# Optimization experiments

Measured on AMD Instinct MI355X. Metric: run time of the kernel, lower is better.

Reference implementation:

```python
import jax, jax.numpy as jnp
import numpy as np

N_NODES = 100000
N_EDGES = 1600000
N_GRAPHS = 512
F_IN = 128
HID = 128
N_CLS = 10


def setup_inputs() -> dict:
    key = jax.random.key(0)
    ks = jax.random.split(key, 8)
    s = 1.0 / np.sqrt(HID)
    x = jax.random.normal(ks[0], (N_NODES, F_IN), dtype=jnp.float32)
    edge_index = jax.random.randint(ks[1], (2, N_EDGES), 0, N_NODES, dtype=jnp.int64)
    batch = jnp.sort(jax.random.randint(ks[2], (N_NODES,), 0, N_GRAPHS, dtype=jnp.int64))
    W0 = jax.random.normal(ks[3], (F_IN, HID), dtype=jnp.float32) * s
    W1 = jax.random.normal(ks[4], (HID, HID), dtype=jnp.float32) * s
    W2 = jax.random.normal(ks[5], (HID, HID), dtype=jnp.float32) * s
    Wl = jax.random.normal(ks[6], (HID, N_CLS), dtype=jnp.float32) * s
    return {
        'x': x, 'edge_index': edge_index, 'batch': batch,
        'W0': W0, 'b0': jnp.zeros((HID,), jnp.float32),
        'W1': W1, 'b1': jnp.zeros((HID,), jnp.float32),
        'W2': W2, 'b2': jnp.zeros((HID,), jnp.float32),
        'Wl': Wl, 'bl': jnp.zeros((N_CLS,), jnp.float32),
    }


def reference(x, edge_index, batch, W0, b0, W1, b1, W2, b2, Wl, bl):
    N = x.shape[0]
    # GCN: add self-loops, symmetric normalization D^-1/2 (A+I) D^-1/2
    loops = jnp.arange(N, dtype=edge_index.dtype)
    row = jnp.concatenate([edge_index[0], loops])  # source
    col = jnp.concatenate([edge_index[1], loops])  # target
    deg = jax.ops.segment_sum(jnp.ones_like(col, dtype=x.dtype), col, num_segments=N)
    dinv = jax.lax.rsqrt(jnp.maximum(deg, 1.0))  # deg >= 1 after self-loops
    norm = dinv[row] * dinv[col]  # [E+N]

    def gcn(h, W, b):
        h = h @ W                       # [N, H] linear transform first (fewer edge flops)
        msg = h[row] * norm[:, None]    # gather + normalize
        return jax.ops.segment_sum(msg, col, num_segments=N) + b  # scatter-add

    h = jax.nn.relu(gcn(x, W0, b0))
    h = jax.nn.relu(gcn(h, W1, b1))
    h = jax.nn.relu(gcn(h, W2, b2))

    # global_mean_pool over graphs
    counts = jax.ops.segment_sum(jnp.ones((N,), x.dtype), batch, num_segments=N_GRAPHS)
    pooled = jax.ops.segment_sum(h, batch, num_segments=N_GRAPHS) / jnp.maximum(counts, 1.0)[:, None]
    return pooled @ Wl + bl
```

## Files before the change

kernel.cpp:

```cpp
#include <hip/hip_runtime.h>
#include <hip/hip_bf16.h>

#define ELL_D 64

typedef __attribute__((ext_vector_type(8))) short short8;
typedef __attribute__((ext_vector_type(4))) float f32x4;

__device__ __forceinline__ unsigned short f2bf(float f) {
    __hip_bfloat16 h = __float2bfloat16(f);
    return *(unsigned short*)&h;
}
__device__ __forceinline__ float bf2f(unsigned short u) {
    unsigned int v = ((unsigned int)u) << 16;
    return __uint_as_float(v);
}


__device__ __forceinline__ void gemm_body(int bid, const float* __restrict__ H,
                                          const float* __restrict__ W, unsigned short* __restrict__ A,
                                          int N, float4* wl4) {
    int tid = threadIdx.x;
    const float4* __restrict__ W4 = (const float4*)W;
    int tc = tid & 15;
    int tr = tid >> 4;
    int rbase = bid * 64 + tr * 4;

    const float4* __restrict__ H4 = (const float4*)H;
    float acc[4][8] = {};
    int r[4];
#pragma unroll
    for (int j = 0; j < 4; j++) {
        int rr = rbase + j;
        r[j] = (rr < N) ? rr : (N - 1);
    }

    for (int p = 0; p < 2; p++) {
        if (p) __syncthreads();
#pragma unroll
        for (int i = 0; i < 8; i++) wl4[i * 256 + tid] = W4[p * 2048 + i * 256 + tid];
        __syncthreads();
#pragma unroll 4
        for (int k4 = 0; k4 < 16; k4++) {
            union { float4 v; float f[4]; } hu[4];
#pragma unroll
            for (int j = 0; j < 4; j++) hu[j].v = H4[r[j] * 32 + p * 16 + k4];
#pragma unroll
            for (int kk = 0; kk < 4; kk++) {
                float4 w0 = wl4[(k4 * 4 + kk) * 32 + tc];
                float4 w1 = wl4[(k4 * 4 + kk) * 32 + 16 + tc];
#pragma unroll
                for (int j = 0; j < 4; j++) {
                    float h = hu[j].f[kk];
                    acc[j][0] = fmaf(h, w0.x, acc[j][0]);
                    acc[j][1] = fmaf(h, w0.y, acc[j][1]);
                    acc[j][2] = fmaf(h, w0.z, acc[j][2]);
                    acc[j][3] = fmaf(h, w0.w, acc[j][3]);
                    acc[j][4] = fmaf(h, w1.x, acc[j][4]);
                    acc[j][5] = fmaf(h, w1.y, acc[j][5]);
                    acc[j][6] = fmaf(h, w1.z, acc[j][6]);
                    acc[j][7] = fmaf(h, w1.w, acc[j][7]);
                }
            }
        }
    }

    ushort4* __restrict__ A4 = (ushort4*)A;
#pragma unroll
    for (int j = 0; j < 4; j++) {
        int rr = rbase + j;
        if (rr < N) {
            A4[rr * 32 + tc]      = make_ushort4(f2bf(acc[j][0]), f2bf(acc[j][1]), f2bf(acc[j][2]), f2bf(acc[j][3]));
            A4[rr * 32 + 16 + tc] = make_ushort4(f2bf(acc[j][4]), f2bf(acc[j][5]), f2bf(acc[j][6]), f2bf(acc[j][7]));
        }
    }
}

__device__ __forceinline__ void fill_body(int bid, const int* __restrict__ col, const int* __restrict__ row,
                                          int* __restrict__ cnt, int* __restrict__ ell, int E) {
    int t = bid * 256 + threadIdx.x;
    int base = t * 4;
    if (base + 4 <= E) {
        int4 c4 = *(const int4*)(col + base);
        int4 r4 = *(const int4*)(row + base);
        int p0 = atomicAdd(&cnt[c4.x], 1) & 63;
        int p1 = atomicAdd(&cnt[c4.y], 1) & 63;
        int p2 = atomicAdd(&cnt[c4.z], 1) & 63;
        int p3 = atomicAdd(&cnt[c4.w], 1) & 63;
        ell[c4.x * ELL_D + p0] = r4.x;
        ell[c4.y * ELL_D + p1] = r4.y;
        ell[c4.z * ELL_D + p2] = r4.z;
        ell[c4.w * ELL_D + p3] = r4.w;
    } else {
        for (int e = base; e < E; e++) {
            int c = col[e];
            int pos = atomicAdd(&cnt[c], 1) & 63;
            ell[c * ELL_D + pos] = row[e];
        }
    }
}

__global__ __launch_bounds__(256) void k_fused_gemm_fill(const float* __restrict__ H, const float* __restrict__ W,
                                                         unsigned short* __restrict__ A,
                                                         const int* __restrict__ col, const int* __restrict__ row,
                                                         int* __restrict__ cnt, int* __restrict__ ell,
                                                         int N, int E, int gb, int fb) {
    __shared__ float4 wl4[2048];
    int half = blockIdx.x >> 1;
    if (!(blockIdx.x & 1)) {
        if (half < gb) gemm_body(half, H, W, A, N, wl4);
    } else {
        if (half < fb) fill_body(half, col, row, cnt, ell, E);
    }
}

__global__ __launch_bounds__(256) void k_prep_wt(const float* __restrict__ W1, const float* __restrict__ W2,
                                                 unsigned short* __restrict__ WT1, unsigned short* __restrict__ WT2) {
    const float* W = blockIdx.x ? W2 : W1;
    unsigned short* WT = blockIdx.x ? WT2 : WT1;
    for (int i = threadIdx.x; i < 16384; i += 256) {
        int c = i >> 7, k = i & 127;
        WT[i] = f2bf(W[k * 128 + c]);
    }
}

__global__ __launch_bounds__(256) void k_dinv_scaleA(const int* __restrict__ cnt, float* __restrict__ dinv,
                                                     unsigned short* __restrict__ A, int N) {
    int node = blockIdx.x * 8 + (threadIdx.x >> 5);
    int li = threadIdx.x & 31;
    if (node >= N) return;
    float dn = 1.0f / sqrtf((float)(cnt[node] + 1));
    if (li == 0) dinv[node] = dn;
    ushort4* Ap = (ushort4*)A + (size_t)node * 32 + li;
    ushort4 v = *Ap;
    v.x = f2bf(bf2f(v.x) * dn);
    v.y = f2bf(bf2f(v.y) * dn);
    v.z = f2bf(bf2f(v.z) * dn);
    v.w = f2bf(bf2f(v.w) * dn);
    *Ap = v;
}


__global__ __launch_bounds__(256) void k_gemm_mfma(const unsigned short* __restrict__ H,
                                                   const unsigned short* __restrict__ WT,
                                                   const float* __restrict__ dinv,
                                                   unsigned short* __restrict__ A, int N) {
    __shared__ float ep[4 * 16 * 132];
    int tid = threadIdx.x, w = tid >> 6, l = tid & 63;
    int rbase = blockIdx.x * 64 + w * 16;
    int lrow = l & 15, lk = l >> 4;

    int r = rbase + lrow;
    if (r >= N) r = N - 1;
    const short8* __restrict__ Hp = (const short8*)(H + (size_t)r * 128);
    short8 af[4];
#pragma unroll
    for (int kc = 0; kc < 4; kc++) af[kc] = Hp[kc * 4 + lk];

    f32x4 acc[8];
#pragma unroll
    for (int t = 0; t < 8; t++) {
        f32x4 a = {0.f, 0.f, 0.f, 0.f};
        const short8* __restrict__ Wp = (const short8*)(WT + (size_t)(t * 16 + lrow) * 128);
#pragma unroll
        for (int kc = 0; kc < 4; kc++) {
            short8 bf = Wp[kc * 4 + lk];
            a = __builtin_amdgcn_mfma_f32_16x16x32_bf16(af[kc], bf, a, 0, 0, 0);
        }
        acc[t] = a;
    }

    float* base = ep + w * 2112;
#pragma unroll
    for (int t = 0; t < 8; t++)
#pragma unroll
        for (int j = 0; j < 4; j++)
            base[(4 * lk + j) * 132 + t * 16 + lrow] = acc[t][j];
    __syncthreads();

    int row16 = l >> 2, c0 = (l & 3) * 32;
    int orow = rbase + row16;
    if (orow < N) {
        float dn = dinv[orow];
        const float* src = base + row16 * 132 + c0;
        unsigned short* dst = A + (size_t)orow * 128 + c0;
#pragma unroll
        for (int q = 0; q < 4; q++) {
            union { short8 s; unsigned short u[8]; } pk;
#pragma unroll
            for (int e = 0; e < 8; e++) pk.u[e] = f2bf(src[q * 8 + e] * dn);
            *(short8*)(dst + q * 8) = pk.s;
        }
    }
}


__global__ __launch_bounds__(256) void k_agg(const unsigned short* __restrict__ A, const int* __restrict__ cnt,
                                             const int* __restrict__ ell, const float* __restrict__ dinv,
                                             const float* __restrict__ bias, unsigned short* __restrict__ Bout, int N) {
    int wid = blockIdx.x * 4 + (threadIdx.x >> 6);
    int lane = threadIdx.x & 63;
    if (wid >= N) return;
    int hi = lane >> 5, li = lane & 31;
    const ushort4* __restrict__ A4 = (const ushort4*)A;
    int deg = cnt[wid];
    float dn = dinv[wid];
    const int* __restrict__ lst = ell + wid * ELL_D;

    int total = deg + 1;
    int pairs = (total + 1) >> 1;

    float4 a0 = {0,0,0,0}, a1 = {0,0,0,0}, a2 = {0,0,0,0}, a3 = {0,0,0,0};
    int i = 0;
    for (; i + 4 <= pairs; i += 4) {
        int s0 = 2 * i + hi, s1 = s0 + 2, s2 = s0 + 4, s3 = s0 + 6;
        int e0 = (s0 < deg) ? lst[s0] : wid;
        int e1 = (s1 < deg) ? lst[s1] : wid;
        int e2 = (s2 < deg) ? lst[s2] : wid;
        int e3 = (s3 < deg) ? lst[s3] : wid;
        float m0 = (s0 < total) ? 1.f : 0.f;
        float m1 = (s1 < total) ? 1.f : 0.f;
        float m2 = (s2 < total) ? 1.f : 0.f;
        float m3 = (s3 < total) ? 1.f : 0.f;
        ushort4 v0 = A4[e0 * 32 + li];
        ushort4 v1 = A4[e1 * 32 + li];
        ushort4 v2 = A4[e2 * 32 + li];
        ushort4 v3 = A4[e3 * 32 + li];
        a0.x = fmaf(bf2f(v0.x), m0, a0.x); a0.y = fmaf(bf2f(v0.y), m0, a0.y);
        a0.z = fmaf(bf2f(v0.z), m0, a0.z); a0.w = fmaf(bf2f(v0.w), m0, a0.w);
        a1.x = fmaf(bf2f(v1.x), m1, a1.x); a1.y = fmaf(bf2f(v1.y), m1, a1.y);
        a1.z = fmaf(bf2f(v1.z), m1, a1.z); a1.w = fmaf(bf2f(v1.w), m1, a1.w);
        a2.x = fmaf(bf2f(v2.x), m2, a2.x); a2.y = fmaf(bf2f(v2.y), m2, a2.y);
        a2.z = fmaf(bf2f(v2.z), m2, a2.z); a2.w = fmaf(bf2f(v2.w), m2, a2.w);
        a3.x = fmaf(bf2f(v3.x), m3, a3.x); a3.y = fmaf(bf2f(v3.y), m3, a3.y);
        a3.z = fmaf(bf2f(v3.z), m3, a3.z); a3.w = fmaf(bf2f(v3.w), m3, a3.w);
    }
    for (; i < pairs; i++) {
        int s0 = 2 * i + hi;
        int e0 = (s0 < deg) ? lst[s0] : wid;
        float m0 = (s0 < total) ? 1.f : 0.f;
        ushort4 v0 = A4[e0 * 32 + li];
        a0.x = fmaf(bf2f(v0.x), m0, a0.x); a0.y = fmaf(bf2f(v0.y), m0, a0.y);
        a0.z = fmaf(bf2f(v0.z), m0, a0.z); a0.w = fmaf(bf2f(v0.w), m0, a0.w);
    }
    a0.x = (a0.x + a1.x) + (a2.x + a3.x);
    a0.y = (a0.y + a1.y) + (a2.y + a3.y);
    a0.z = (a0.z + a1.z) + (a2.z + a3.z);
    a0.w = (a0.w + a1.w) + (a2.w + a3.w);
    a0.x += __shfl_xor(a0.x, 32, 64);
    a0.y += __shfl_xor(a0.y, 32, 64);
    a0.z += __shfl_xor(a0.z, 32, 64);
    a0.w += __shfl_xor(a0.w, 32, 64);

    if (hi == 0) {
        const float4* __restrict__ b4 = (const float4*)bias;
        float4 bb = b4[li];
        ushort4 o;
        o.x = f2bf(fmaxf(fmaf(a0.x, dn, bb.x), 0.f));
        o.y = f2bf(fmaxf(fmaf(a0.y, dn, bb.y), 0.f));
        o.z = f2bf(fmaxf(fmaf(a0.z, dn, bb.z), 0.f));
        o.w = f2bf(fmaxf(fmaf(a0.w, dn, bb.w), 0.f));
        ((ushort4*)Bout)[wid * 32 + li] = o;
    }
}


__global__ __launch_bounds__(512) void k_pool(const unsigned short* __restrict__ B, const int* __restrict__ batch,
                                              const float* __restrict__ Wl, const float* __restrict__ bl,
                                              float* __restrict__ out, int N) {
    int g = blockIdx.x;
    int tid = threadIdx.x;
    int k = tid & 127, h = tid >> 7;
    __shared__ int se[2];
    __shared__ float red[4][128];
    if (tid < 2) {
        int target = g + tid;
        int lo = 0, hi = N;
        while (lo < hi) {
            int mid = (lo + hi) >> 1;
            if (batch[mid] < target) lo = mid + 1; else hi = mid;
        }
        se[tid] = lo;
    }
    __syncthreads();
    int start = se[0], end = se[1];
    float s = 0.f;
    for (int n = start + h; n < end; n += 4) s += bf2f(B[n * 128 + k]);
    red[h][k] = s;
    __syncthreads();
    if (h == 0) {
        float tot = red[0][k] + red[1][k] + red[2][k] + red[3][k];
        int cg = end - start;
        red[0][k] = tot / (float)(cg > 1 ? cg : 1);
    }
    __syncthreads();
    if (tid < 10) {
        float o = bl[tid];
        for (int j = 0; j < 128; j++) o = fmaf(red[0][j], Wl[j * 10 + tid], o);
        out[g * 10 + tid] = o;
    }
}


extern "C" void kernel_launch(void* const* d_in, const int* in_sizes, int n_in,
                              void* d_out, int out_size, void* d_ws, size_t ws_size,
                              hipStream_t stream) {
    const float* x  = (const float*)d_in[0];
    const int* eidx = (const int*)d_in[1];
    const int* batch = (const int*)d_in[2];
    const float* W0 = (const float*)d_in[3];
    const float* b0 = (const float*)d_in[4];
    const float* W1 = (const float*)d_in[5];
    const float* b1 = (const float*)d_in[6];
    const float* W2 = (const float*)d_in[7];
    const float* b2 = (const float*)d_in[8];
    const float* Wl = (const float*)d_in[9];
    const float* bl = (const float*)d_in[10];

    int N = in_sizes[0] / 128;
    int E = in_sizes[1] / 2;
    int G = out_size / 10;
    const int* row = eidx;
    const int* col = eidx + E;

    char* w = (char*)d_ws;
    auto carve = [&](size_t bytes) -> void* {
        void* p = (void*)w;
        w += (bytes + 511) & ~(size_t)511;
        return p;
    };
    unsigned short* A  = (unsigned short*)carve((size_t)N * 128 * 2);
    unsigned short* Bb = (unsigned short*)carve((size_t)N * 128 * 2);
    int*   cnt  = (int*)carve((size_t)N * 4);
    float* dinv = (float*)carve((size_t)N * 4);
    int*   ell  = (int*)carve((size_t)N * ELL_D * 4);
    unsigned short* WT1 = (unsigned short*)carve(16384 * 2);
    unsigned short* WT2 = (unsigned short*)carve(16384 * 2);

    int gb = (N + 63) / 64;
    int ft = (E + 3) / 4;
    int fb = (ft + 255) / 256;
    int M  = (gb > fb) ? gb : fb;

    hipMemsetAsync(cnt, 0, (size_t)N * 4, stream);
    k_prep_wt<<<2, 256, 0, stream>>>(W1, W2, WT1, WT2);
    k_fused_gemm_fill<<<2 * M, 256, 0, stream>>>(x, W0, A, col, row, cnt, ell, N, E, gb, fb);
    k_dinv_scaleA<<<(N + 7) / 8, 256, 0, stream>>>(cnt, dinv, A, N);

    int ab = (N + 3) / 4;
    int mb = (N + 63) / 64;
    k_agg<<<ab, 256, 0, stream>>>(A, cnt, ell, dinv, b0, Bb, N);
    k_gemm_mfma<<<mb, 256, 0, stream>>>(Bb, WT1, dinv, A, N);
    k_agg<<<ab, 256, 0, stream>>>(A, cnt, ell, dinv, b1, Bb, N);
    k_gemm_mfma<<<mb, 256, 0, stream>>>(Bb, WT2, dinv, A, N);
    k_agg<<<ab, 256, 0, stream>>>(A, cnt, ell, dinv, b2, Bb, N);
    k_pool<<<G, 512, 0, stream>>>(Bb, batch, Wl, bl, (float*)d_out, N);
}
```

Before: 411.9 us.

## Partition ELL fill by destination range across block groups for atomic locality

```diff
diff --git a/kernel.cpp b/kernel.cpp
--- a/kernel.cpp
+++ b/kernel.cpp
@@ -2,6 +2,8 @@
 #include <hip/hip_bf16.h>
 
 #define ELL_D 64
+#define FK 128
+#define FBT (8 * FK)
 
 typedef __attribute__((ext_vector_type(8))) short short8;
 typedef __attribute__((ext_vector_type(4))) float f32x4;
@@ -75,41 +77,49 @@
     }
 }
 
-__device__ __forceinline__ void fill_body(int bid, const int* __restrict__ col, const int* __restrict__ row,
-                                          int* __restrict__ cnt, int* __restrict__ ell, int E) {
-    int t = bid * 256 + threadIdx.x;
-    int base = t * 4;
-    if (base + 4 <= E) {
-        int4 c4 = *(const int4*)(col + base);
-        int4 r4 = *(const int4*)(row + base);
-        int p0 = atomicAdd(&cnt[c4.x], 1) & 63;
-        int p1 = atomicAdd(&cnt[c4.y], 1) & 63;
-        int p2 = atomicAdd(&cnt[c4.z], 1) & 63;
-        int p3 = atomicAdd(&cnt[c4.w], 1) & 63;
-        ell[c4.x * ELL_D + p0] = r4.x;
-        ell[c4.y * ELL_D + p1] = r4.y;
-        ell[c4.z * ELL_D + p2] = r4.z;
-        ell[c4.w * ELL_D + p3] = r4.w;
+
+__device__ __forceinline__ void fill_own_body(int b, const int* __restrict__ col, const int* __restrict__ row,
+                                              int* __restrict__ cnt, int* __restrict__ ell, int E, int N) {
+    int r = b & 7, k = b >> 3;
+    int nr = (N + 7) / 8;
+    int lo = r * nr;
+    int hi = lo + nr; if (hi > N) hi = N;
+    int tid = threadIdx.x;
+    int E4 = E >> 2;
+    int chunk = (E4 + FK - 1) / FK;
+    int q0 = k * chunk;
+    int q1 = q0 + chunk; if (q1 > E4) q1 = E4;
+    const int4* __restrict__ c4p = (const int4*)col;
+    const int4* __restrict__ r4p = (const int4*)row;
+    for (int q = q0 + tid; q < q1; q += 256) {
+        int4 c4 = c4p[q];
+        int4 r4 = r4p[q];
+        if (c4.x >= lo && c4.x < hi) { int p = atomicAdd(&cnt[c4.x], 1) & 63; ell[c4.x * ELL_D + p] = r4.x; }
+        if (c4.y >= lo && c4.y < hi) { int p = atomicAdd(&cnt[c4.y], 1) & 63; ell[c4.y * ELL_D + p] = r4.y; }
+        if (c4.z >= lo && c4.z < hi) { int p = atomicAdd(&cnt[c4.z], 1) & 63; ell[c4.z * ELL_D + p] = r4.z; }
+        if (c4.w >= lo && c4.w < hi) { int p = atomicAdd(&cnt[c4.w], 1) & 63; ell[c4.w * ELL_D + p] = r4.w; }
+    }
+    if (k == FK - 1) {
+        int rem = E & 3;
+        if (tid < rem) {
+            int e = E4 * 4 + tid;
+            int c = col[e];
+            if (c >= lo && c < hi) { int p = atomicAdd(&cnt[c], 1) & 63; ell[c * ELL_D + p] = row[e]; }
+        }
+    }
+}
+
+__global__ __launch_bounds__(256) void k_fused(const float* __restrict__ H, const float* __restrict__ W,
+                                               unsigned short* __restrict__ A,
+                                               const int* __restrict__ col, const int* __restrict__ row,
+                                               int* __restrict__ cnt, int* __restrict__ ell,
+                                               int N, int E, int gb) {
+    __shared__ float4 wl4[2048];
+    if (blockIdx.x < FBT) {
+        fill_own_body(blockIdx.x, col, row, cnt, ell, E, N);
     } else {
-        for (int e = base; e < E; e++) {
-            int c = col[e];
-            int pos = atomicAdd(&cnt[c], 1) & 63;
-            ell[c * ELL_D + pos] = row[e];
-        }
-    }
-}
-
-__global__ __launch_bounds__(256) void k_fused_gemm_fill(const float* __restrict__ H, const float* __restrict__ W,
-                                                         unsigned short* __restrict__ A,
-                                                         const int* __restrict__ col, const int* __restrict__ row,
-                                                         int* __restrict__ cnt, int* __restrict__ ell,
-                                                         int N, int E, int gb, int fb) {
-    __shared__ float4 wl4[2048];
-    int half = blockIdx.x >> 1;
-    if (!(blockIdx.x & 1)) {
-        if (half < gb) gemm_body(half, H, W, A, N, wl4);
-    } else {
-        if (half < fb) fill_body(half, col, row, cnt, ell, E);
+        int gbid = blockIdx.x - FBT;
+        if (gbid < gb) gemm_body(gbid, H, W, A, N, wl4);
     }
 }
 
@@ -185,10 +195,10 @@
         unsigned short* dst = A + (size_t)orow * 128 + c0;
 #pragma unroll
         for (int q = 0; q < 4; q++) {
-            union { short8 s; unsigned short u[8]; } pk;
+            union { short8 s8; unsigned short u[8]; } pk;
 #pragma unroll
             for (int e = 0; e < 8; e++) pk.u[e] = f2bf(src[q * 8 + e] * dn);
-            *(short8*)(dst + q * 8) = pk.s;
+            *(short8*)(dst + q * 8) = pk.s8;
         }
     }
 }
@@ -337,13 +347,10 @@
     unsigned short* WT2 = (unsigned short*)carve(16384 * 2);
 
     int gb = (N + 63) / 64;
-    int ft = (E + 3) / 4;
-    int fb = (ft + 255) / 256;
-    int M  = (gb > fb) ? gb : fb;
 
     hipMemsetAsync(cnt, 0, (size_t)N * 4, stream);
     k_prep_wt<<<2, 256, 0, stream>>>(W1, W2, WT1, WT2);
-    k_fused_gemm_fill<<<2 * M, 256, 0, stream>>>(x, W0, A, col, row, cnt, ell, N, E, gb, fb);
+    k_fused<<<FBT + gb, 256, 0, stream>>>(x, W0, A, col, row, cnt, ell, N, E, gb);
     k_dinv_scaleA<<<(N + 7) / 8, 256, 0, stream>>>(cnt, dinv, A, N);
 
     int ab = (N + 3) / 4;
```

Measured after the change: 428.2 us. +4.0%, slower.

## Fuse aggregation with next-layer MFMA GEMM and pad ELL lists with sentinel rows

Applied to the files above, without the earlier changes.

```diff
diff --git a/kernel.cpp b/kernel.cpp
--- a/kernel.cpp
+++ b/kernel.cpp
@@ -74,6 +74,7 @@
         }
     }
 }
+
 
 __device__ __forceinline__ void fill_body(int bid, const int* __restrict__ col, const int* __restrict__ row,
                                           int* __restrict__ cnt, int* __restrict__ ell, int E) {
@@ -99,11 +100,11 @@
     }
 }
 
-__global__ __launch_bounds__(256) void k_fused_gemm_fill(const float* __restrict__ H, const float* __restrict__ W,
-                                                         unsigned short* __restrict__ A,
-                                                         const int* __restrict__ col, const int* __restrict__ row,
-                                                         int* __restrict__ cnt, int* __restrict__ ell,
-                                                         int N, int E, int gb, int fb) {
+__global__ __launch_bounds__(256) void k_fused(const float* __restrict__ H, const float* __restrict__ W,
+                                               unsigned short* __restrict__ A,
+                                               const int* __restrict__ col, const int* __restrict__ row,
+                                               int* __restrict__ cnt, int* __restrict__ ell,
+                                               int N, int E, int gb, int fb) {
     __shared__ float4 wl4[2048];
     int half = blockIdx.x >> 1;
     if (!(blockIdx.x & 1)) {
@@ -123,44 +124,128 @@
     }
 }
 
-__global__ __launch_bounds__(256) void k_dinv_scaleA(const int* __restrict__ cnt, float* __restrict__ dinv,
-                                                     unsigned short* __restrict__ A, int N) {
+
+__global__ __launch_bounds__(256) void k_scaleA_pad(const int* __restrict__ cnt, float* __restrict__ dinv,
+                                                    unsigned short* __restrict__ A1, unsigned short* __restrict__ A2,
+                                                    int* __restrict__ ell, int N) {
     int node = blockIdx.x * 8 + (threadIdx.x >> 5);
     int li = threadIdx.x & 31;
-    if (node >= N) return;
-    float dn = 1.0f / sqrtf((float)(cnt[node] + 1));
-    if (li == 0) dinv[node] = dn;
-    ushort4* Ap = (ushort4*)A + (size_t)node * 32 + li;
-    ushort4 v = *Ap;
-    v.x = f2bf(bf2f(v.x) * dn);
-    v.y = f2bf(bf2f(v.y) * dn);
-    v.z = f2bf(bf2f(v.z) * dn);
-    v.w = f2bf(bf2f(v.w) * dn);
-    *Ap = v;
-}
-
-
-__global__ __launch_bounds__(256) void k_gemm_mfma(const unsigned short* __restrict__ H,
-                                                   const unsigned short* __restrict__ WT,
-                                                   const float* __restrict__ dinv,
-                                                   unsigned short* __restrict__ A, int N) {
-    __shared__ float ep[4 * 16 * 132];
+    if (node < N) {
+        int deg = cnt[node];
+        float dn = 1.0f / sqrtf((float)(deg + 1));
+        if (deg > 63) deg = 63;
+        if (li == 0) dinv[node] = dn;
+        ushort4* Ap = (ushort4*)A1 + (size_t)node * 32 + li;
+        ushort4 v = *Ap;
+        v.x = f2bf(bf2f(v.x) * dn);
+        v.y = f2bf(bf2f(v.y) * dn);
+        v.z = f2bf(bf2f(v.z) * dn);
+        v.w = f2bf(bf2f(v.w) * dn);
+        *Ap = v;
+        int pend = (deg + 4) & ~3;
+        int* er = ell + (size_t)node * ELL_D;
+        if (li == 0) er[deg] = node;
+        else if (li < 4 && deg + li < pend) er[deg + li] = N;
+    }
+    if (blockIdx.x == 0) {
+        int t = threadIdx.x;
+        if (t < 64) {
+            ushort4 z = make_ushort4(0, 0, 0, 0);
+            if (t < 32) ((ushort4*)A1)[(size_t)N * 32 + t] = z;
+            else        ((ushort4*)A2)[(size_t)N * 32 + (t - 32)] = z;
+        }
+    }
+}
+
+
+__device__ __forceinline__ void agg_core(const ushort4* __restrict__ A4r, const int* __restrict__ cnt,
+                                         const int* __restrict__ ell, int n, int hi, int li,
+                                         float4& a0, float4& a1) {
+    int deg = cnt[n];
+    if (deg > 63) deg = 63;
+    int nq = (deg + 4) >> 2;
+    const int4* __restrict__ l4 = (const int4*)(ell + (size_t)n * ELL_D);
+    int q = 0;
+    for (; q + 2 <= nq; q += 2) {
+        int4 qa = l4[q], qb = l4[q + 1];
+        int e0 = hi ? qa.y : qa.x, e1 = hi ? qa.w : qa.z;
+        int e2 = hi ? qb.y : qb.x, e3 = hi ? qb.w : qb.z;
+        ushort4 v0 = A4r[(size_t)e0 * 32 + li];
+        ushort4 v1 = A4r[(size_t)e1 * 32 + li];
+        ushort4 v2 = A4r[(size_t)e2 * 32 + li];
+        ushort4 v3 = A4r[(size_t)e3 * 32 + li];
+        a0.x += bf2f(v0.x) + bf2f(v1.x);
+        a0.y += bf2f(v0.y) + bf2f(v1.y);
+        a0.z += bf2f(v0.z) + bf2f(v1.z);
+        a0.w += bf2f(v0.w) + bf2f(v1.w);
+        a1.x += bf2f(v2.x) + bf2f(v3.x);
+        a1.y += bf2f(v2.y) + bf2f(v3.y);
+        a1.z += bf2f(v2.z) + bf2f(v3.z);
+        a1.w += bf2f(v2.w) + bf2f(v3.w);
+    }
+    if (q < nq) {
+        int4 qa = l4[q];
+        int e0 = hi ? qa.y : qa.x, e1 = hi ? qa.w : qa.z;
+        ushort4 v0 = A4r[(size_t)e0 * 32 + li];
+        ushort4 v1 = A4r[(size_t)e1 * 32 + li];
+        a0.x += bf2f(v0.x) + bf2f(v1.x);
+        a0.y += bf2f(v0.y) + bf2f(v1.y);
+        a0.z += bf2f(v0.z) + bf2f(v1.z);
+        a0.w += bf2f(v0.w) + bf2f(v1.w);
+    }
+}
+
+
+__global__ __launch_bounds__(256) void k_agg_gemm(const unsigned short* __restrict__ Ain,
+                                                  const int* __restrict__ cnt, const int* __restrict__ ell,
+                                                  const float* __restrict__ dinv, const float* __restrict__ bias,
+                                                  const unsigned short* __restrict__ WT,
+                                                  unsigned short* __restrict__ Aout, int N) {
+    __shared__ char lds[33792];
+    unsigned short* hb = (unsigned short*)lds;
+    float* ep = (float*)lds;
     int tid = threadIdx.x, w = tid >> 6, l = tid & 63;
-    int rbase = blockIdx.x * 64 + w * 16;
-    int lrow = l & 15, lk = l >> 4;
-
-    int r = rbase + lrow;
-    if (r >= N) r = N - 1;
-    const short8* __restrict__ Hp = (const short8*)(H + (size_t)r * 128);
+    int hi = l >> 5, li = l & 31;
+    int rbase = blockIdx.x * 64;
+    const ushort4* __restrict__ A4r = (const ushort4*)Ain;
+    float4 bb = ((const float4*)bias)[li];
+
+    for (int it = 0; it < 16; ++it) {
+        int lrow = w * 16 + it;
+        int n = rbase + lrow;
+        float4 a0 = {0, 0, 0, 0}, a1 = {0, 0, 0, 0};
+        if (n < N) {
+            agg_core(A4r, cnt, ell, n, hi, li, a0, a1);
+            a0.x += a1.x; a0.y += a1.y; a0.z += a1.z; a0.w += a1.w;
+            a0.x += __shfl_xor(a0.x, 32, 64);
+            a0.y += __shfl_xor(a0.y, 32, 64);
+            a0.z += __shfl_xor(a0.z, 32, 64);
+            a0.w += __shfl_xor(a0.w, 32, 64);
+        }
+        if (hi == 0) {
+            float dn = (n < N) ? dinv[n] : 0.f;
+            ushort4 o;
+            o.x = f2bf(fmaxf(fmaf(a0.x, dn, bb.x), 0.f));
+            o.y = f2bf(fmaxf(fmaf(a0.y, dn, bb.y), 0.f));
+            o.z = f2bf(fmaxf(fmaf(a0.z, dn, bb.z), 0.f));
+            o.w = f2bf(fmaxf(fmaf(a0.w, dn, bb.w), 0.f));
+            *(ushort4*)(hb + (size_t)lrow * 136 + li * 4) = o;
+        }
+    }
+    __syncthreads();
+
+    int lrow16 = l & 15, lk = l >> 4;
+    const unsigned short* hrow = hb + (size_t)(w * 16 + lrow16) * 136;
     short8 af[4];
 #pragma unroll
-    for (int kc = 0; kc < 4; kc++) af[kc] = Hp[kc * 4 + lk];
+    for (int kc = 0; kc < 4; kc++) af[kc] = *(const short8*)(hrow + kc * 32 + lk * 8);
+    __syncthreads();
 
     f32x4 acc[8];
 #pragma unroll
     for (int t = 0; t < 8; t++) {
         f32x4 a = {0.f, 0.f, 0.f, 0.f};
-        const short8* __restrict__ Wp = (const short8*)(WT + (size_t)(t * 16 + lrow) * 128);
+        const short8* __restrict__ Wp = (const short8*)(WT + (size_t)(t * 16 + lrow16) * 128);
 #pragma unroll
         for (int kc = 0; kc < 4; kc++) {
             short8 bf = Wp[kc * 4 + lk];
@@ -174,86 +259,44 @@
     for (int t = 0; t < 8; t++)
 #pragma unroll
         for (int j = 0; j < 4; j++)
-            base[(4 * lk + j) * 132 + t * 16 + lrow] = acc[t][j];
+            base[(4 * lk + j) * 132 + t * 16 + lrow16] = acc[t][j];
     __syncthreads();
 
     int row16 = l >> 2, c0 = (l & 3) * 32;
-    int orow = rbase + row16;
+    int orow = rbase + w * 16 + row16;
     if (orow < N) {
         float dn = dinv[orow];
         const float* src = base + row16 * 132 + c0;
-        unsigned short* dst = A + (size_t)orow * 128 + c0;
+        unsigned short* dst = Aout + (size_t)orow * 128 + c0;
 #pragma unroll
         for (int q = 0; q < 4; q++) {
-            union { short8 s; unsigned short u[8]; } pk;
+            union { short8 s8; unsigned short u[8]; } pk;
 #pragma unroll
             for (int e = 0; e < 8; e++) pk.u[e] = f2bf(src[q * 8 + e] * dn);
-            *(short8*)(dst + q * 8) = pk.s;
-        }
-    }
-}
-
-
-__global__ __launch_bounds__(256) void k_agg(const unsigned short* __restrict__ A, const int* __restrict__ cnt,
+            *(short8*)(dst + q * 8) = pk.s8;
+        }
+    }
+}
+
+
+__global__ __launch_bounds__(256) void k_agg(const unsigned short* __restrict__ Ain, const int* __restrict__ cnt,
                                              const int* __restrict__ ell, const float* __restrict__ dinv,
                                              const float* __restrict__ bias, unsigned short* __restrict__ Bout, int N) {
     int wid = blockIdx.x * 4 + (threadIdx.x >> 6);
     int lane = threadIdx.x & 63;
     if (wid >= N) return;
     int hi = lane >> 5, li = lane & 31;
-    const ushort4* __restrict__ A4 = (const ushort4*)A;
-    int deg = cnt[wid];
-    float dn = dinv[wid];
-    const int* __restrict__ lst = ell + wid * ELL_D;
-
-    int total = deg + 1;
-    int pairs = (total + 1) >> 1;
-
-    float4 a0 = {0,0,0,0}, a1 = {0,0,0,0}, a2 = {0,0,0,0}, a3 = {0,0,0,0};
-    int i = 0;
-    for (; i + 4 <= pairs; i += 4) {
-        int s0 = 2 * i + hi, s1 = s0 + 2, s2 = s0 + 4, s3 = s0 + 6;
-        int e0 = (s0 < deg) ? lst[s0] : wid;
-        int e1 = (s1 < deg) ? lst[s1] : wid;
-        int e2 = (s2 < deg) ? lst[s2] : wid;
-        int e3 = (s3 < deg) ? lst[s3] : wid;
-        float m0 = (s0 < total) ? 1.f : 0.f;
-        float m1 = (s1 < total) ? 1.f : 0.f;
-        float m2 = (s2 < total) ? 1.f : 0.f;
-        float m3 = (s3 < total) ? 1.f : 0.f;
-        ushort4 v0 = A4[e0 * 32 + li];
-        ushort4 v1 = A4[e1 * 32 + li];
-        ushort4 v2 = A4[e2 * 32 + li];
-        ushort4 v3 = A4[e3 * 32 + li];
-        a0.x = fmaf(bf2f(v0.x), m0, a0.x); a0.y = fmaf(bf2f(v0.y), m0, a0.y);
-        a0.z = fmaf(bf2f(v0.z), m0, a0.z); a0.w = fmaf(bf2f(v0.w), m0, a0.w);
-        a1.x = fmaf(bf2f(v1.x), m1, a1.x); a1.y = fmaf(bf2f(v1.y), m1, a1.y);
-        a1.z = fmaf(bf2f(v1.z), m1, a1.z); a1.w = fmaf(bf2f(v1.w), m1, a1.w);
-        a2.x = fmaf(bf2f(v2.x), m2, a2.x); a2.y = fmaf(bf2f(v2.y), m2, a2.y);
-        a2.z = fmaf(bf2f(v2.z), m2, a2.z); a2.w = fmaf(bf2f(v2.w), m2, a2.w);
-        a3.x = fmaf(bf2f(v3.x), m3, a3.x); a3.y = fmaf(bf2f(v3.y), m3, a3.y);
-        a3.z = fmaf(bf2f(v3.z), m3, a3.z); a3.w = fmaf(bf2f(v3.w), m3, a3.w);
-    }
-    for (; i < pairs; i++) {
-        int s0 = 2 * i + hi;
-        int e0 = (s0 < deg) ? lst[s0] : wid;
-        float m0 = (s0 < total) ? 1.f : 0.f;
-        ushort4 v0 = A4[e0 * 32 + li];
-        a0.x = fmaf(bf2f(v0.x), m0, a0.x); a0.y = fmaf(bf2f(v0.y), m0, a0.y);
-        a0.z = fmaf(bf2f(v0.z), m0, a0.z); a0.w = fmaf(bf2f(v0.w), m0, a0.w);
-    }
-    a0.x = (a0.x + a1.x) + (a2.x + a3.x);
-    a0.y = (a0.y + a1.y) + (a2.y + a3.y);
-    a0.z = (a0.z + a1.z) + (a2.z + a3.z);
-    a0.w = (a0.w + a1.w) + (a2.w + a3.w);
+    const ushort4* __restrict__ A4r = (const ushort4*)Ain;
+    float4 a0 = {0, 0, 0, 0}, a1 = {0, 0, 0, 0};
+    agg_core(A4r, cnt, ell, wid, hi, li, a0, a1);
+    a0.x += a1.x; a0.y += a1.y; a0.z += a1.z; a0.w += a1.w;
     a0.x += __shfl_xor(a0.x, 32, 64);
     a0.y += __shfl_xor(a0.y, 32, 64);
     a0.z += __shfl_xor(a0.z, 32, 64);
     a0.w += __shfl_xor(a0.w, 32, 64);
-
     if (hi == 0) {
-        const float4* __restrict__ b4 = (const float4*)bias;
-        float4 bb = b4[li];
+        float dn = dinv[wid];
+        float4 bb = ((const float4*)bias)[li];
         ushort4 o;
         o.x = f2bf(fmaxf(fmaf(a0.x, dn, bb.x), 0.f));
         o.y = f2bf(fmaxf(fmaf(a0.y, dn, bb.y), 0.f));
@@ -328,7 +371,8 @@
         w += (bytes + 511) & ~(size_t)511;
         return p;
     };
-    unsigned short* A  = (unsigned short*)carve((size_t)N * 128 * 2);
+    unsigned short* A1 = (unsigned short*)carve((size_t)(N + 1) * 128 * 2);
+    unsigned short* A2 = (unsigned short*)carve((size_t)(N + 1) * 128 * 2);
     unsigned short* Bb = (unsigned short*)carve((size_t)N * 128 * 2);
     int*   cnt  = (int*)carve((size_t)N * 4);
     float* dinv = (float*)carve((size_t)N * 4);
@@ -343,15 +387,12 @@
 
     hipMemsetAsync(cnt, 0, (size_t)N * 4, stream);
     k_prep_wt<<<2, 256, 0, stream>>>(W1, W2, WT1, WT2);
-    k_fused_gemm_fill<<<2 * M, 256, 0, stream>>>(x, W0, A, col, row, cnt, ell, N, E, gb, fb);
-    k_dinv_scaleA<<<(N + 7) / 8, 256, 0, stream>>>(cnt, dinv, A, N);
-
-    int ab = (N + 3) / 4;
+    k_fused<<<2 * M, 256, 0, stream>>>(x, W0, A1, col, row, cnt, ell, N, E, gb, fb);
+    k_scaleA_pad<<<(N + 7) / 8, 256, 0, stream>>>(cnt, dinv, A1, A2, ell, N);
+
     int mb = (N + 63) / 64;
-    k_agg<<<ab, 256, 0, stream>>>(A, cnt, ell, dinv, b0, Bb, N);
-    k_gemm_mfma<<<mb, 256, 0, stream>>>(Bb, WT1, dinv, A, N);
-    k_agg<<<ab, 256, 0, stream>>>(A, cnt, ell, dinv, b1, Bb, N);
-    k_gemm_mfma<<<mb, 256, 0, stream>>>(Bb, WT2, dinv, A, N);
-    k_agg<<<ab, 256, 0, stream>>>(A, cnt, ell, dinv, b2, Bb, N);
+    k_agg_gemm<<<mb, 256, 0, stream>>>(A1, cnt, ell, dinv, b0, WT1, A2, N);
+    k_agg_gemm<<<mb, 256, 0, stream>>>(A2, cnt, ell, dinv, b1, WT2, A1, N);
+    k_agg<<<(N + 3) / 4, 256, 0, stream>>>(A1, cnt, ell, dinv, b2, Bb, N);
     k_pool<<<G, 512, 0, stream>>>(Bb, batch, Wl, bl, (float*)d_out, N);
 }
```

After: 451.3 us. 9.6% more time.

## Pad ELL rows with self-loop and zero-row sentinel; half-wave-per-node aggregation

Applied to the files above, without the earlier changes.

```diff
diff --git a/kernel.cpp b/kernel.cpp
--- a/kernel.cpp
+++ b/kernel.cpp
@@ -74,6 +74,7 @@
         }
     }
 }
+
 
 __device__ __forceinline__ void fill_body(int bid, const int* __restrict__ col, const int* __restrict__ row,
                                           int* __restrict__ cnt, int* __restrict__ ell, int E) {
@@ -99,11 +100,11 @@
     }
 }
 
-__global__ __launch_bounds__(256) void k_fused_gemm_fill(const float* __restrict__ H, const float* __restrict__ W,
-                                                         unsigned short* __restrict__ A,
-                                                         const int* __restrict__ col, const int* __restrict__ row,
-                                                         int* __restrict__ cnt, int* __restrict__ ell,
-                                                         int N, int E, int gb, int fb) {
+__global__ __launch_bounds__(256) void k_fused(const float* __restrict__ H, const float* __restrict__ W,
+                                               unsigned short* __restrict__ A,
+                                               const int* __restrict__ col, const int* __restrict__ row,
+                                               int* __restrict__ cnt, int* __restrict__ ell,
+                                               int N, int E, int gb, int fb) {
     __shared__ float4 wl4[2048];
     int half = blockIdx.x >> 1;
     if (!(blockIdx.x & 1)) {
@@ -123,20 +124,78 @@
     }
 }
 
-__global__ __launch_bounds__(256) void k_dinv_scaleA(const int* __restrict__ cnt, float* __restrict__ dinv,
-                                                     unsigned short* __restrict__ A, int N) {
+
+__global__ __launch_bounds__(256) void k_scaleA_pad(const int* __restrict__ cnt, float* __restrict__ dinv,
+                                                    unsigned short* __restrict__ A, int* __restrict__ ell, int N) {
     int node = blockIdx.x * 8 + (threadIdx.x >> 5);
     int li = threadIdx.x & 31;
-    if (node >= N) return;
-    float dn = 1.0f / sqrtf((float)(cnt[node] + 1));
-    if (li == 0) dinv[node] = dn;
-    ushort4* Ap = (ushort4*)A + (size_t)node * 32 + li;
-    ushort4 v = *Ap;
-    v.x = f2bf(bf2f(v.x) * dn);
-    v.y = f2bf(bf2f(v.y) * dn);
-    v.z = f2bf(bf2f(v.z) * dn);
-    v.w = f2bf(bf2f(v.w) * dn);
-    *Ap = v;
+    if (node < N) {
+        int deg = cnt[node];
+        float dn = 1.0f / sqrtf((float)(deg + 1));
+        if (deg > 63) deg = 63;
+        if (li == 0) dinv[node] = dn;
+        ushort4* Ap = (ushort4*)A + (size_t)node * 32 + li;
+        ushort4 v = *Ap;
+        v.x = f2bf(bf2f(v.x) * dn);
+        v.y = f2bf(bf2f(v.y) * dn);
+        v.z = f2bf(bf2f(v.z) * dn);
+        v.w = f2bf(bf2f(v.w) * dn);
+        *Ap = v;
+        int pend = (deg + 8) & ~7;
+        if (pend > 64) pend = 64;
+        int* er = ell + (size_t)node * ELL_D;
+        if (li == 0) er[deg] = node;
+        else if (li < 8 && deg + li < pend) er[deg + li] = N;
+    }
+    if (blockIdx.x == 0 && threadIdx.x < 32) {
+        ((ushort4*)A)[(size_t)N * 32 + threadIdx.x] = make_ushort4(0, 0, 0, 0);
+    }
+}
+
+
+__global__ __launch_bounds__(256) void k_agg(const unsigned short* __restrict__ Ain, const int* __restrict__ cnt,
+                                             const int* __restrict__ ell, const float* __restrict__ dinv,
+                                             const float* __restrict__ bias, unsigned short* __restrict__ Bout, int N) {
+    int lane = threadIdx.x & 63;
+    int hi = lane >> 5, li = lane & 31;
+    int n = blockIdx.x * 8 + ((threadIdx.x >> 6) << 1) + hi;
+    if (n >= N) return;
+    const ushort4* __restrict__ A4r = (const ushort4*)Ain;
+    int deg = cnt[n];
+    if (deg > 63) deg = 63;
+    int pend = (deg + 8) & ~7;
+    if (pend > 64) pend = 64;
+    int nq = pend >> 2;
+    const int4* __restrict__ l4 = (const int4*)(ell + (size_t)n * ELL_D);
+
+    float4 a0 = {0, 0, 0, 0}, a1 = {0, 0, 0, 0};
+    for (int q = 0; q < nq; q += 2) {
+        int4 qa = l4[q], qb = l4[q + 1];
+        ushort4 v0 = A4r[(size_t)qa.x * 32 + li];
+        ushort4 v1 = A4r[(size_t)qa.y * 32 + li];
+        ushort4 v2 = A4r[(size_t)qa.z * 32 + li];
+        ushort4 v3 = A4r[(size_t)qa.w * 32 + li];
+        ushort4 v4 = A4r[(size_t)qb.x * 32 + li];
+        ushort4 v5 = A4r[(size_t)qb.y * 32 + li];
+        ushort4 v6 = A4r[(size_t)qb.z * 32 + li];
+        ushort4 v7 = A4r[(size_t)qb.w * 32 + li];
+        a0.x += (bf2f(v0.x) + bf2f(v1.x)) + (bf2f(v2.x) + bf2f(v3.x));
+        a0.y += (bf2f(v0.y) + bf2f(v1.y)) + (bf2f(v2.y) + bf2f(v3.y));
+        a0.z += (bf2f(v0.z) + bf2f(v1.z)) + (bf2f(v2.z) + bf2f(v3.z));
+        a0.w += (bf2f(v0.w) + bf2f(v1.w)) + (bf2f(v2.w) + bf2f(v3.w));
+        a1.x += (bf2f(v4.x) + bf2f(v5.x)) + (bf2f(v6.x) + bf2f(v7.x));
+        a1.y += (bf2f(v4.y) + bf2f(v5.y)) + (bf2f(v6.y) + bf2f(v7.y));
+        a1.z += (bf2f(v4.z) + bf2f(v5.z)) + (bf2f(v6.z) + bf2f(v7.z));
+        a1.w += (bf2f(v4.w) + bf2f(v5.w)) + (bf2f(v6.w) + bf2f(v7.w));
+    }
+    float dn = dinv[n];
+    float4 bb = ((const float4*)bias)[li];
+    ushort4 o;
+    o.x = f2bf(fmaxf(fmaf(a0.x + a1.x, dn, bb.x), 0.f));
+    o.y = f2bf(fmaxf(fmaf(a0.y + a1.y, dn, bb.y), 0.f));
+    o.z = f2bf(fmaxf(fmaf(a0.z + a1.z, dn, bb.z), 0.f));
+    o.w = f2bf(fmaxf(fmaf(a0.w + a1.w, dn, bb.w), 0.f));
+    ((ushort4*)Bout)[(size_t)n * 32 + li] = o;
 }
 
 
@@ -185,81 +244,11 @@
         unsigned short* dst = A + (size_t)orow * 128 + c0;
 #pragma unroll
         for (int q = 0; q < 4; q++) {
-            union { short8 s; unsigned short u[8]; } pk;
+            union { short8 s8; unsigned short u[8]; } pk;
 #pragma unroll
             for (int e = 0; e < 8; e++) pk.u[e] = f2bf(src[q * 8 + e] * dn);
-            *(short8*)(dst + q * 8) = pk.s;
-        }
-    }
-}
-
-
-__global__ __launch_bounds__(256) void k_agg(const unsigned short* __restrict__ A, const int* __restrict__ cnt,
-                                             const int* __restrict__ ell, const float* __restrict__ dinv,
-                                             const float* __restrict__ bias, unsigned short* __restrict__ Bout, int N) {
-    int wid = blockIdx.x * 4 + (threadIdx.x >> 6);
-    int lane = threadIdx.x & 63;
-    if (wid >= N) return;
-    int hi = lane >> 5, li = lane & 31;
-    const ushort4* __restrict__ A4 = (const ushort4*)A;
-    int deg = cnt[wid];
-    float dn = dinv[wid];
-    const int* __restrict__ lst = ell + wid * ELL_D;
-
-    int total = deg + 1;
-    int pairs = (total + 1) >> 1;
-
-    float4 a0 = {0,0,0,0}, a1 = {0,0,0,0}, a2 = {0,0,0,0}, a3 = {0,0,0,0};
-    int i = 0;
-    for (; i + 4 <= pairs; i += 4) {
-        int s0 = 2 * i + hi, s1 = s0 + 2, s2 = s0 + 4, s3 = s0 + 6;
-        int e0 = (s0 < deg) ? lst[s0] : wid;
-        int e1 = (s1 < deg) ? lst[s1] : wid;
-        int e2 = (s2 < deg) ? lst[s2] : wid;
-        int e3 = (s3 < deg) ? lst[s3] : wid;
-        float m0 = (s0 < total) ? 1.f : 0.f;
-        float m1 = (s1 < total) ? 1.f : 0.f;
-        float m2 = (s2 < total) ? 1.f : 0.f;
-        float m3 = (s3 < total) ? 1.f : 0.f;
-        ushort4 v0 = A4[e0 * 32 + li];
-        ushort4 v1 = A4[e1 * 32 + li];
-        ushort4 v2 = A4[e2 * 32 + li];
-        ushort4 v3 = A4[e3 * 32 + li];
-        a0.x = fmaf(bf2f(v0.x), m0, a0.x); a0.y = fmaf(bf2f(v0.y), m0, a0.y);
-        a0.z = fmaf(bf2f(v0.z), m0, a0.z); a0.w = fmaf(bf2f(v0.w), m0, a0.w);
-        a1.x = fmaf(bf2f(v1.x), m1, a1.x); a1.y = fmaf(bf2f(v1.y), m1, a1.y);
-        a1.z = fmaf(bf2f(v1.z), m1, a1.z); a1.w = fmaf(bf2f(v1.w), m1, a1.w);
-        a2.x = fmaf(bf2f(v2.x), m2, a2.x); a2.y = fmaf(bf2f(v2.y), m2, a2.y);
-        a2.z = fmaf(bf2f(v2.z), m2, a2.z); a2.w = fmaf(bf2f(v2.w), m2, a2.w);
-        a3.x = fmaf(bf2f(v3.x), m3, a3.x); a3.y = fmaf(bf2f(v3.y), m3, a3.y);
-        a3.z = fmaf(bf2f(v3.z), m3, a3.z); a3.w = fmaf(bf2f(v3.w), m3, a3.w);
-    }
-    for (; i < pairs; i++) {
-        int s0 = 2 * i + hi;
-        int e0 = (s0 < deg) ? lst[s0] : wid;
-        float m0 = (s0 < total) ? 1.f : 0.f;
-        ushort4 v0 = A4[e0 * 32 + li];
-        a0.x = fmaf(bf2f(v0.x), m0, a0.x); a0.y = fmaf(bf2f(v0.y), m0, a0.y);
-        a0.z = fmaf(bf2f(v0.z), m0, a0.z); a0.w = fmaf(bf2f(v0.w), m0, a0.w);
-    }
-    a0.x = (a0.x + a1.x) + (a2.x + a3.x);
-    a0.y = (a0.y + a1.y) + (a2.y + a3.y);
-    a0.z = (a0.z + a1.z) + (a2.z + a3.z);
-    a0.w = (a0.w + a1.w) + (a2.w + a3.w);
-    a0.x += __shfl_xor(a0.x, 32, 64);
-    a0.y += __shfl_xor(a0.y, 32, 64);
-    a0.z += __shfl_xor(a0.z, 32, 64);
-    a0.w += __shfl_xor(a0.w, 32, 64);
-
-    if (hi == 0) {
-        const float4* __restrict__ b4 = (const float4*)bias;
-        float4 bb = b4[li];
-        ushort4 o;
-        o.x = f2bf(fmaxf(fmaf(a0.x, dn, bb.x), 0.f));
-        o.y = f2bf(fmaxf(fmaf(a0.y, dn, bb.y), 0.f));
-        o.z = f2bf(fmaxf(fmaf(a0.z, dn, bb.z), 0.f));
-        o.w = f2bf(fmaxf(fmaf(a0.w, dn, bb.w), 0.f));
-        ((ushort4*)Bout)[wid * 32 + li] = o;
+            *(short8*)(dst + q * 8) = pk.s8;
+        }
     }
 }
 
@@ -328,7 +317,7 @@
         w += (bytes + 511) & ~(size_t)511;
         return p;
     };
-    unsigned short* A  = (unsigned short*)carve((size_t)N * 128 * 2);
+    unsigned short* A  = (unsigned short*)carve((size_t)(N + 1) * 128 * 2);
     unsigned short* Bb = (unsigned short*)carve((size_t)N * 128 * 2);
     int*   cnt  = (int*)carve((size_t)N * 4);
     float* dinv = (float*)carve((size_t)N * 4);
@@ -343,10 +332,10 @@
 
     hipMemsetAsync(cnt, 0, (size_t)N * 4, stream);
     k_prep_wt<<<2, 256, 0, stream>>>(W1, W2, WT1, WT2);
-    k_fused_gemm_fill<<<2 * M, 256, 0, stream>>>(x, W0, A, col, row, cnt, ell, N, E, gb, fb);
-    k_dinv_scaleA<<<(N + 7) / 8, 256, 0, stream>>>(cnt, dinv, A, N);
-
-    int ab = (N + 3) / 4;
+    k_fused<<<2 * M, 256, 0, stream>>>(x, W0, A, col, row, cnt, ell, N, E, gb, fb);
+    k_scaleA_pad<<<(N + 7) / 8, 256, 0, stream>>>(cnt, dinv, A, ell, N);
+
+    int ab = (N + 7) / 8;
     int mb = (N + 63) / 64;
     k_agg<<<ab, 256, 0, stream>>>(A, cnt, ell, dinv, b0, Bb, N);
     k_gemm_mfma<<<mb, 256, 0, stream>>>(Bb, WT1, dinv, A, N);
```

New measurement: 396.2 us. -3.8%, faster.
